# Optimization experiments

Measured on AMD Instinct MI355X. Metric: run time of the kernel, lower is better.

The kernel has to match this reference:

```python
import jax, jax.numpy as jnp
import numpy as np

_SAMPLING_EPS = 1e-5


def setup_inputs() -> dict:
    key = jax.random.key(0)
    k1, k2, k3, k4, k5 = jax.random.split(key, 5)
    B, V = 128, 128000
    logits = jax.random.normal(k1, (B, V), dtype=jnp.float32)
    temperature = jax.random.uniform(k2, (B,), dtype=jnp.float32)  # some rows < eps -> greedy
    top_k = jax.random.randint(k3, (B,), 1, 64, dtype=jnp.int32)   # in [1, 63]
    top_p = jax.random.uniform(k4, (B,), dtype=jnp.float32, minval=0.05, maxval=1.0)
    noise_u = jax.random.uniform(k5, (B, V), dtype=jnp.float32, minval=1e-10, maxval=1.0)
    return {"logits": logits, "temperature": temperature, "top_k": top_k,
            "top_p": top_p, "noise_u": noise_u, "max_num_logprobs": 5}


def _apply_top_k_top_p(logits, k, p):
    # Faithful to vLLM: ascending sort, top-k threshold mask, top-p cumsum mask, scatter back.
    B, V = logits.shape
    order = jnp.argsort(logits, axis=-1)                       # ascending, [B, V]
    logits_sort = jnp.take_along_axis(logits, order, axis=-1)
    neg_inf = jnp.float32(-jnp.inf)
    # top-k: pivot value at position V - k; everything strictly below it -> -inf
    pivot_idx = (V - k.astype(jnp.int32))[:, None]             # [B, 1]
    pivot = jnp.take_along_axis(logits_sort, pivot_idx, axis=-1)
    logits_sort = jnp.where(logits_sort < pivot, neg_inf, logits_sort)
    # top-p: softmax over sorted logits, cumsum, drop prefix with mass <= 1 - p (keep last)
    probs_sort = jax.nn.softmax(logits_sort, axis=-1)
    probs_sum = jnp.cumsum(probs_sort, axis=-1)
    top_p_mask = probs_sum <= (1.0 - p)[:, None]
    top_p_mask = top_p_mask.at[:, -1].set(False)
    logits_sort = jnp.where(top_p_mask, neg_inf, logits_sort)
    # scatter back to original vocab order
    rows = jnp.arange(B)[:, None]
    return jnp.zeros_like(logits).at[rows, order].set(logits_sort)


def reference(logits, temperature, top_k, top_p, noise_u, max_num_logprobs):
    # temperature scaling (temp < eps means greedy; divide by 1.0 instead)
    temp = jnp.where(temperature < _SAMPLING_EPS, 1.0, temperature)
    logits = logits.astype(jnp.float32) / temp[:, None]
    # top-k / top-p filtering
    logits = _apply_top_k_top_p(logits, top_k, top_p)
    # probabilities and sampling
    probs = jax.nn.softmax(logits, axis=-1)
    greedy = jnp.argmax(probs, axis=-1)
    q = -jnp.log(noise_u)                                      # Exp(1) noise (q.exponential_())
    random = jnp.argmax(probs / q, axis=-1)
    sampled = jnp.where(temperature < _SAMPLING_EPS, greedy, random).astype(jnp.int32)
    # top-k logprobs
    logprobs = jax.nn.log_softmax(logits, axis=-1)
    topk_logprobs, topk_indices = jax.lax.top_k(logprobs, max_num_logprobs)
    return sampled, topk_indices.astype(jnp.int32), topk_logprobs
```

## Files before the change

kernel.cpp:

```cpp
#include <hip/hip_runtime.h>
#include <math.h>
#include <stdint.h>

#define BT     256
#define WPB    4
#define TOPC   64
#define CAPW   1024
#define WT     512
#define NSL_HI 32
#define NSL_LO 16
#define NC_MAX (NSL_HI * TOPC)

__device__ __forceinline__ unsigned f2ord(float f) {
    unsigned u = __float_as_uint(f);
    return u ^ ((u & 0x80000000u) ? 0xFFFFFFFFu : 0x80000000u);
}
__device__ __forceinline__ float ord2f(unsigned k) {
    unsigned u = (k & 0x80000000u) ? (k ^ 0x80000000u) : (k ^ 0xFFFFFFFFu);
    return __uint_as_float(u);
}

template<int G>
__device__ unsigned wave_rebuild64_g(unsigned* key, int* idx, unsigned n,
                                     int lane, unsigned* out_vst)
{
    unsigned kr[G]; int ir[G];
    #pragma unroll
    for (int g = 0; g < G; ++g) {
        unsigned i = (unsigned)(g * 64 + lane);
        kr[g] = (i < n) ? key[i] : 0u;
        ir[g] = (i < n) ? idx[i] : 0;
    }
    unsigned p = 0u;
    for (int bit = 31; bit >= 0; --bit) {
        unsigned t = p | (1u << bit);
        int c = 0;
        #pragma unroll
        for (int g = 0; g < G; ++g)
            c += __popcll(__ballot(kr[g] >= t));
        if (c >= TOPC) p = t;
    }
    const unsigned long long ltm = (1ull << lane) - 1ull;
    unsigned c = 0;
    #pragma unroll
    for (int g = 0; g < G; ++g) {
        unsigned i = (unsigned)(g * 64 + lane);
        bool pa = (i < n) && (kr[g] > p);
        unsigned long long m = __ballot(pa);
        if (pa) { unsigned pos = c + (unsigned)__popcll(m & ltm); key[pos] = kr[g]; idx[pos] = ir[g]; }
        c += (unsigned)__popcll(m);
    }
    #pragma unroll
    for (int g = 0; g < G; ++g) {
        unsigned i = (unsigned)(g * 64 + lane);
        bool pa = (i < n) && (kr[g] == p);
        unsigned long long m = __ballot(pa);
        if (pa) {
            unsigned pos = c + (unsigned)__popcll(m & ltm);
            if (pos < TOPC) { key[pos] = kr[g]; idx[pos] = ir[g]; }
        }
        c += (unsigned)__popcll(m);
    }
    *out_vst = p;
    return (c < TOPC) ? c : TOPC;
}

__device__ __forceinline__ unsigned wave_rebuild64(unsigned* key, int* idx,
                                                   unsigned n, int lane,
                                                   unsigned* out_vst)
{
    if (n <= 256)  return wave_rebuild64_g<4>(key, idx, n, lane, out_vst);
    if (n <= 512)  return wave_rebuild64_g<8>(key, idx, n, lane, out_vst);
    return wave_rebuild64_g<16>(key, idx, n, lane, out_vst);
}

__global__ __launch_bounds__(BT) void phase1_topk_slices(
    const float* __restrict__ logits, uint2* __restrict__ cand,
    int V, int slice_len, int nsl)
{
    __shared__ unsigned s_key[WPB][CAPW];
    __shared__ int      s_idx[WPB][CAPW];

    const int row  = blockIdx.y;
    const int tid  = threadIdx.x;
    const int wid  = tid >> 6;
    const int lane = tid & 63;
    const int sl   = blockIdx.x * WPB + wid;
    const int s0   = sl * slice_len;
    int s_end = s0 + slice_len; if (s_end > V) s_end = V;
    const float* rowp = logits + (size_t)row * (size_t)V;
    unsigned* mykey = s_key[wid];
    int*      myidx = s_idx[wid];
    const unsigned long long ltm = (1ull << lane) - 1ull;

    const int  tb0 = s0 + 0 * WT + lane * 8, tb1 = s0 + 1 * WT + lane * 8;
    const int  tb2 = s0 + 2 * WT + lane * 8, tb3 = s0 + 3 * WT + lane * 8;
    const int  tb4 = s0 + 4 * WT + lane * 8, tb5 = s0 + 5 * WT + lane * 8;
    const int  tb6 = s0 + 6 * WT + lane * 8, tb7 = s0 + 7 * WT + lane * 8;
    const bool vt0 = tb0 < s_end, vt1 = tb1 < s_end, vt2 = tb2 < s_end,
               vt3 = tb3 < s_end, vt4 = tb4 < s_end, vt5 = tb5 < s_end,
               vt6 = tb6 < s_end, vt7 = tb7 < s_end;

    float4 sa0 = {}, sb0 = {}, sa1 = {}, sb1 = {};
    if (vt0) { sa0 = *(const float4*)(rowp + tb0); sb0 = *(const float4*)(rowp + tb0 + 4); }
    if (vt1) { sa1 = *(const float4*)(rowp + tb1); sb1 = *(const float4*)(rowp + tb1 + 4); }

    float4 A2 = {}, B2 = {}, A3 = {}, B3 = {};
    float4 A4 = {}, B4 = {}, A5 = {}, B5 = {};
    if (vt2) { A2 = *(const float4*)(rowp + tb2); B2 = *(const float4*)(rowp + tb2 + 4); }
    if (vt3) { A3 = *(const float4*)(rowp + tb3); B3 = *(const float4*)(rowp + tb3 + 4); }
    if (vt4) { A4 = *(const float4*)(rowp + tb4); B4 = *(const float4*)(rowp + tb4 + 4); }
    if (vt5) { A5 = *(const float4*)(rowp + tb5); B5 = *(const float4*)(rowp + tb5 + 4); }

    unsigned k0[8], k1[8];
    if (vt0) {
        k0[0] = f2ord(sa0.x); k0[1] = f2ord(sa0.y); k0[2] = f2ord(sa0.z); k0[3] = f2ord(sa0.w);
        k0[4] = f2ord(sb0.x); k0[5] = f2ord(sb0.y); k0[6] = f2ord(sb0.z); k0[7] = f2ord(sb0.w);
    } else {
        #pragma unroll
        for (int j = 0; j < 8; ++j) k0[j] = 0u;
    }
    if (vt1) {
        k1[0] = f2ord(sa1.x); k1[1] = f2ord(sa1.y); k1[2] = f2ord(sa1.z); k1[3] = f2ord(sa1.w);
        k1[4] = f2ord(sb1.x); k1[5] = f2ord(sb1.y); k1[6] = f2ord(sb1.z); k1[7] = f2ord(sb1.w);
    } else {
        #pragma unroll
        for (int j = 0; j < 8; ++j) k1[j] = 0u;
    }

    unsigned lo = 0u, hi = 0xFFFFu;
    while (lo < hi) {
        unsigned mid = (lo + hi + 1u) >> 1;
        unsigned t = mid << 16;
        int cnt16 = 0;
        #pragma unroll
        for (int j = 0; j < 8; ++j) {
            cnt16 += __popcll(__ballot(k0[j] >= t));
            cnt16 += __popcll(__ballot(k1[j] >= t));
        }
        if (cnt16 >= TOPC) lo = mid; else hi = mid - 1u;
    }
    const unsigned thr = lo << 16;

    unsigned cnt = 0u;
    auto append8 = [&](const unsigned* k, int base, bool valid) {
        #pragma unroll
        for (int j = 0; j < 8; ++j) {
            bool pa = valid && (k[j] >= thr);
            unsigned long long m = __ballot(pa);
            if (pa) {
                unsigned pos = cnt + (unsigned)__popcll(m & ltm);
                if (pos < CAPW) { mykey[pos] = k[j]; myidx[pos] = base + j; }
            }
            cnt += (unsigned)__popcll(m);
        }
    };
    auto conv8 = [&](unsigned* k, const float4& a, const float4& b, bool valid) {
        if (valid) {
            k[0] = f2ord(a.x); k[1] = f2ord(a.y); k[2] = f2ord(a.z); k[3] = f2ord(a.w);
            k[4] = f2ord(b.x); k[5] = f2ord(b.y); k[6] = f2ord(b.z); k[7] = f2ord(b.w);
        } else {
            #pragma unroll
            for (int j = 0; j < 8; ++j) k[j] = 0u;
        }
    };

    append8(k0, tb0, vt0);
    append8(k1, tb1, vt1);

    {
        unsigned kk[8];
        conv8(kk, A2, B2, vt2);
        if (vt6) { A2 = *(const float4*)(rowp + tb6); B2 = *(const float4*)(rowp + tb6 + 4); }
        append8(kk, tb2, vt2);
    }
    {
        unsigned kk[8];
        conv8(kk, A3, B3, vt3);
        if (vt7) { A3 = *(const float4*)(rowp + tb7); B3 = *(const float4*)(rowp + tb7 + 4); }
        append8(kk, tb3, vt3);
    }
    {   unsigned kk[8]; conv8(kk, A4, B4, vt4); append8(kk, tb4, vt4); }
    {   unsigned kk[8]; conv8(kk, A5, B5, vt5); append8(kk, tb5, vt5); }
    {   unsigned kk[8]; conv8(kk, A2, B2, vt6); append8(kk, tb6, vt6); }
    {   unsigned kk[8]; conv8(kk, A3, B3, vt7); append8(kk, tb7, vt7); }

    for (int t = s0 + 8 * WT; t < s_end; t += WT) {
        int bs = t + lane * 8;
        bool v = bs < s_end;
        float4 aa = {}, bb = {};
        if (v) { aa = *(const float4*)(rowp + bs); bb = *(const float4*)(rowp + bs + 4); }
        unsigned kk[8];
        conv8(kk, aa, bb, v);
        append8(kk, bs, v);
    }

    asm volatile("s_waitcnt lgkmcnt(0)" ::: "memory");
    __builtin_amdgcn_sched_barrier(0);
    unsigned n = cnt;

    if (n > CAPW) {
        unsigned vst;
        cnt = wave_rebuild64_g<16>(mykey, myidx, CAPW, lane, &vst);
        for (int t = s0; t < s_end; t += WT) {
            int bs = t + lane * 8;
            bool v = bs < s_end;
            float4 aa = {}, bb = {};
            if (v) { aa = *(const float4*)(rowp + bs); bb = *(const float4*)(rowp + bs + 4); }
            unsigned kk[8];
            conv8(kk, aa, bb, v);
            for (;;) {
                unsigned long long m[8]; unsigned tot = 0u;
                #pragma unroll
                for (int j = 0; j < 8; ++j) {
                    m[j] = __ballot(v && (kk[j] > vst));
                    tot += (unsigned)__popcll(m[j]);
                }
                if (cnt + tot <= CAPW) {
                    unsigned c2 = cnt;
                    #pragma unroll
                    for (int j = 0; j < 8; ++j) {
                        if (v && (kk[j] > vst)) {
                            unsigned pos = c2 + (unsigned)__popcll(m[j] & ltm);
                            mykey[pos] = kk[j]; myidx[pos] = bs + j;
                        }
                        c2 += (unsigned)__popcll(m[j]);
                    }
                    cnt = c2;
                    break;
                }
                asm volatile("s_waitcnt lgkmcnt(0)" ::: "memory");
                __builtin_amdgcn_sched_barrier(0);
                cnt = wave_rebuild64_g<16>(mykey, myidx, cnt, lane, &vst);
            }
        }
        asm volatile("s_waitcnt lgkmcnt(0)" ::: "memory");
        __builtin_amdgcn_sched_barrier(0);
        n = cnt;
    }

    unsigned vfin;
    unsigned c2 = wave_rebuild64(mykey, myidx, n, lane, &vfin);
    asm volatile("s_waitcnt lgkmcnt(0)" ::: "memory");
    __builtin_amdgcn_sched_barrier(0);

    uint2* outp = cand + ((size_t)row * (unsigned)nsl + (unsigned)sl) * TOPC;
    unsigned e = (unsigned)lane;
    uint2 val = (e < c2) ? make_uint2(mykey[e], (unsigned)myidx[e])
                         : make_uint2(0u, 0u);
    outp[e] = val;
}

__device__ unsigned radix_select_compact4(uint2* s_buf, uint2* s_keep,
                                          unsigned (*s_hist)[16], unsigned* p_cnt2,
                                          unsigned n, int tid, int wid)
{
    unsigned prefix = 0u;
    int remaining = TOPC;
    for (int shift = 28; shift >= 0; shift -= 4) {
        if (tid < 64) ((unsigned*)s_hist)[tid] = 0u;
        __syncthreads();
        for (unsigned i = (unsigned)tid; i < n; i += BT) {
            unsigned k = s_buf[i].x;
            bool ing = (shift == 28) || ((k >> (shift + 4)) == (prefix >> (shift + 4)));
            if (ing) atomicAdd(&s_hist[wid][(k >> shift) & 15u], 1u);
        }
        __syncthreads();
        int cum = 0; int b = 0; unsigned hb = 0u;
        for (int bb = 15; bb >= 0; --bb) {
            unsigned h = s_hist[0][bb] + s_hist[1][bb] + s_hist[2][bb] + s_hist[3][bb];
            cum += (int)h;
            if (cum >= remaining) { b = bb; hb = h; break; }
        }
        remaining -= (cum - (int)hb);
        prefix |= ((unsigned)b) << shift;
        __syncthreads();
    }
    if (tid == 0) *p_cnt2 = 0u;
    __syncthreads();
    for (unsigned i = (unsigned)tid; i < n; i += BT) {
        uint2 c = s_buf[i];
        if (c.x > prefix) s_keep[atomicAdd(p_cnt2, 1u)] = c;
    }
    __syncthreads();
    for (unsigned i = (unsigned)tid; i < n; i += BT) {
        uint2 c = s_buf[i];
        if (c.x == prefix) {
            unsigned pos = atomicAdd(p_cnt2, 1u);
            if (pos < TOPC) s_keep[pos] = c;
        }
    }
    __syncthreads();
    return prefix;
}

__global__ __launch_bounds__(BT) void phase2_sample(
    const uint2* __restrict__ cand,
    const float* __restrict__ temperature,
    const int*   __restrict__ top_k,
    const float* __restrict__ top_p,
    const float* __restrict__ noise_u,
    float* __restrict__ out,
    int B, int V, int M, int nc)
{
    __shared__ uint2    s_buf[NC_MAX];
    __shared__ uint2    s_keep[TOPC];
    __shared__ unsigned s_hist[4][16];
    __shared__ unsigned s_cnt2;
    __shared__ float    sval[TOPC], se[TOPC], sq[TOPC];
    __shared__ int      sidx[TOPC];

    const int r   = blockIdx.x;
    const int tid = threadIdx.x;
    const int wid = tid >> 6;

    for (int i = tid; i < nc; i += BT)
        s_buf[i] = cand[(size_t)r * nc + i];
    __syncthreads();
    radix_select_compact4(s_buf, s_keep, s_hist, &s_cnt2, (unsigned)nc, tid, wid);

    for (int kk = 2; kk <= TOPC; kk <<= 1) {
        for (int j = kk >> 1; j > 0; j >>= 1) {
            if (tid < TOPC / 2) {
                int i0 = ((tid & ~(j - 1)) << 1) | (tid & (j - 1));
                int i1 = i0 | j;
                bool up = ((i0 & kk) == 0);
                uint2 A = s_keep[i0], Bv = s_keep[i1];
                bool gt = (A.x < Bv.x) || (A.x == Bv.x && A.y > Bv.y);
                if (gt == up) { s_keep[i0] = Bv; s_keep[i1] = A; }
            }
            __syncthreads();
        }
    }

    float temp_orig = temperature[r];
    float temp = (temp_orig < 1e-5f) ? 1.0f : temp_orig;

    if (tid < TOPC) {
        unsigned k = s_keep[tid].x;
        int id = (int)s_keep[tid].y;
        sval[tid] = ord2f(k) / temp;
        sidx[tid] = id;
        float u = noise_u[(size_t)r * (size_t)V + id];
        sq[tid] = -logf(u);
    }
    __syncthreads();
    if (tid < TOPC) se[tid] = expf(sval[tid] - sval[0]);
    __syncthreads();

    if (tid == 0) {
        int k = top_k[r];
        if (k < 1) k = 1; if (k > TOPC) k = TOPC;
        float p = top_p[r];

        float pivot = sval[k - 1];
        int m = k;
        while (m < TOPC && sval[m] >= pivot) ++m;

        float sum = 0.f;
        for (int i = 0; i < m; ++i) sum += se[i];

        float thr1 = 1.0f - p;
        float S = 0.f;
        int f = 1;
        for (int i = m - 1; i >= 1; --i) {
            S += se[i] / sum;
            if (S > thr1) { f = i + 1; break; }
        }

        float sum2 = 0.f;
        for (int i = 0; i < f; ++i) sum2 += se[i];

        int greedy = sidx[0];
        float best = -1.f; int bidx = 0x7fffffff;
        for (int i = 0; i < f; ++i) {
            float ratio = (se[i] / sum2) / sq[i];
            if (ratio > best || (ratio == best && sidx[i] < bidx)) {
                best = ratio; bidx = sidx[i];
            }
        }
        int sampled = (temp_orig < 1e-5f) ? greedy : bidx;

        float lse = logf(sum2);
        out[r] = (float)sampled;
        float* oidx = out + B + (size_t)r * M;
        float* olp  = out + B + (size_t)B * M + (size_t)r * M;
        int produced = 0;
        for (int i = 0; i < f && produced < M; ++i, ++produced) {
            oidx[produced] = (float)sidx[i];
            olp[produced]  = (sval[i] - sval[0]) - lse;
        }
        int v = 0;
        while (produced < M) {
            bool used = false;
            for (int i = 0; i < f; ++i) if (sidx[i] == v) { used = true; break; }
            if (!used) { oidx[produced] = (float)v; olp[produced] = -3.0e38f; ++produced; }
            ++v;
        }
    }
}

extern "C" void kernel_launch(void* const* d_in, const int* in_sizes, int n_in,
                              void* d_out, int out_size, void* d_ws, size_t ws_size,
                              hipStream_t stream)
{
    const float* logits      = (const float*)d_in[0];
    const float* temperature = (const float*)d_in[1];
    const int*   top_k       = (const int*)d_in[2];
    const float* top_p       = (const float*)d_in[3];
    const float* noise_u     = (const float*)d_in[4];

    const int B = in_sizes[1];
    const int V = in_sizes[0] / B;
    const int M = (out_size / B - 1) / 2;

    const size_t need32 = (size_t)B * NSL_HI * TOPC * sizeof(uint2);
    const int nsl = (ws_size >= need32) ? NSL_HI : NSL_LO;

    uint2* cand = (uint2*)d_ws;

    int slice_len = (((V + nsl - 1) / nsl) + 7) & ~7;

    dim3 g1(nsl / WPB, B);
    phase1_topk_slices<<<g1, BT, 0, stream>>>(logits, cand, V, slice_len, nsl);
    phase2_sample<<<B, BT, 0, stream>>>(cand, temperature, top_k, top_p, noise_u,
                                        (float*)d_out, B, V, M, nsl * TOPC);
}
```

Baseline: 180.0 us.

## Stream logits through an LDS ring with async global-to-LDS loads in phase 1

Phase 1 now pulls each slice through an 8-stage per-wave LDS ring using global_load_lds async copies, with vmcnt waits, instead of register-held float4 prefetches. The aim is to keep more memory requests in flight while the threshold and append work runs. Slice count drops from 32 to 24 and candidate capacity from 1024 to 640, which frees LDS for the ring and shrinks phase-2 input. Some lgkmcnt waits around the rebuilds are removed. This risks hazards between LDS reads and writes, and the larger per-wave slices give less grid parallelism.

```diff
diff --git a/kernel.cpp b/kernel.cpp
--- a/kernel.cpp
+++ b/kernel.cpp
@@ -5,11 +5,13 @@
 #define BT     256
 #define WPB    4
 #define TOPC   64
-#define CAPW   1024
+#define CAPW   640
+#define SUB    256
+#define RING   8
 #define WT     512
-#define NSL_HI 32
-#define NSL_LO 16
-#define NC_MAX (NSL_HI * TOPC)
+#define NSL_HI 24
+#define NSL_LO 8
+#define NC_MAX 2048
 
 __device__ __forceinline__ unsigned f2ord(float f) {
     unsigned u = __float_as_uint(f);
@@ -19,6 +21,14 @@
     unsigned u = (k & 0x80000000u) ? (k ^ 0x80000000u) : (k ^ 0xFFFFFFFFu);
     return __uint_as_float(u);
 }
+
+__device__ __forceinline__ void async_copy16(const float* gsrc, unsigned* lds) {
+    __builtin_amdgcn_global_load_lds(
+        (const __attribute__((address_space(1))) void*)gsrc,
+        (__attribute__((address_space(3))) void*)lds, 16, 0, 0);
+}
+#define WAITV(N) do { asm volatile("s_waitcnt vmcnt(" #N ")" ::: "memory"); \
+                      __builtin_amdgcn_sched_barrier(0); } while (0)
 
 template<int G>
 __device__ unsigned wave_rebuild64_g(unsigned* key, int* idx, unsigned n,
@@ -64,20 +74,20 @@
     *out_vst = p;
     return (c < TOPC) ? c : TOPC;
 }
-
 __device__ __forceinline__ unsigned wave_rebuild64(unsigned* key, int* idx,
                                                    unsigned n, int lane,
                                                    unsigned* out_vst)
 {
-    if (n <= 256)  return wave_rebuild64_g<4>(key, idx, n, lane, out_vst);
-    if (n <= 512)  return wave_rebuild64_g<8>(key, idx, n, lane, out_vst);
-    return wave_rebuild64_g<16>(key, idx, n, lane, out_vst);
+    if (n <= 256) return wave_rebuild64_g<4>(key, idx, n, lane, out_vst);
+    if (n <= 512) return wave_rebuild64_g<8>(key, idx, n, lane, out_vst);
+    return wave_rebuild64_g<12>(key, idx, n, lane, out_vst);
 }
 
 __global__ __launch_bounds__(BT) void phase1_topk_slices(
     const float* __restrict__ logits, uint2* __restrict__ cand,
     int V, int slice_len, int nsl)
 {
+    __shared__ unsigned s_ring[WPB][RING * SUB];
     __shared__ unsigned s_key[WPB][CAPW];
     __shared__ int      s_idx[WPB][CAPW];
 
@@ -89,64 +99,65 @@
     const int s0   = sl * slice_len;
     int s_end = s0 + slice_len; if (s_end > V) s_end = V;
     const float* rowp = logits + (size_t)row * (size_t)V;
+    unsigned* ring  = s_ring[wid];
     unsigned* mykey = s_key[wid];
     int*      myidx = s_idx[wid];
     const unsigned long long ltm = (1ull << lane) - 1ull;
-
-    const int  tb0 = s0 + 0 * WT + lane * 8, tb1 = s0 + 1 * WT + lane * 8;
-    const int  tb2 = s0 + 2 * WT + lane * 8, tb3 = s0 + 3 * WT + lane * 8;
-    const int  tb4 = s0 + 4 * WT + lane * 8, tb5 = s0 + 5 * WT + lane * 8;
-    const int  tb6 = s0 + 6 * WT + lane * 8, tb7 = s0 + 7 * WT + lane * 8;
-    const bool vt0 = tb0 < s_end, vt1 = tb1 < s_end, vt2 = tb2 < s_end,
-               vt3 = tb3 < s_end, vt4 = tb4 < s_end, vt5 = tb5 < s_end,
-               vt6 = tb6 < s_end, vt7 = tb7 < s_end;
-
-    float4 sa0 = {}, sb0 = {}, sa1 = {}, sb1 = {};
-    if (vt0) { sa0 = *(const float4*)(rowp + tb0); sb0 = *(const float4*)(rowp + tb0 + 4); }
-    if (vt1) { sa1 = *(const float4*)(rowp + tb1); sb1 = *(const float4*)(rowp + tb1 + 4); }
-
-    float4 A2 = {}, B2 = {}, A3 = {}, B3 = {};
-    float4 A4 = {}, B4 = {}, A5 = {}, B5 = {};
-    if (vt2) { A2 = *(const float4*)(rowp + tb2); B2 = *(const float4*)(rowp + tb2 + 4); }
-    if (vt3) { A3 = *(const float4*)(rowp + tb3); B3 = *(const float4*)(rowp + tb3 + 4); }
-    if (vt4) { A4 = *(const float4*)(rowp + tb4); B4 = *(const float4*)(rowp + tb4 + 4); }
-    if (vt5) { A5 = *(const float4*)(rowp + tb5); B5 = *(const float4*)(rowp + tb5 + 4); }
-
-    unsigned k0[8], k1[8];
-    if (vt0) {
-        k0[0] = f2ord(sa0.x); k0[1] = f2ord(sa0.y); k0[2] = f2ord(sa0.z); k0[3] = f2ord(sa0.w);
-        k0[4] = f2ord(sb0.x); k0[5] = f2ord(sb0.y); k0[6] = f2ord(sb0.z); k0[7] = f2ord(sb0.w);
-    } else {
-        #pragma unroll
-        for (int j = 0; j < 8; ++j) k0[j] = 0u;
-    }
-    if (vt1) {
-        k1[0] = f2ord(sa1.x); k1[1] = f2ord(sa1.y); k1[2] = f2ord(sa1.z); k1[3] = f2ord(sa1.w);
-        k1[4] = f2ord(sb1.x); k1[5] = f2ord(sb1.y); k1[6] = f2ord(sb1.z); k1[7] = f2ord(sb1.w);
-    } else {
-        #pragma unroll
-        for (int j = 0; j < 8; ++j) k1[j] = 0u;
+    const int lane4 = lane * 4;
+
+    uint2* outp = cand + ((size_t)row * (unsigned)nsl + (unsigned)sl) * TOPC;
+
+    const int NSUB = (s_end > s0) ? ((s_end - s0 + SUB - 1) / SUB) : 0;
+    if (NSUB <= 0) {
+        outp[lane] = make_uint2(0u, 0u);
+        return;
+    }
+    const int vclamp = V - 4;
+
+    auto issue = [&](int st) {
+        int off = s0 + st * SUB + lane4;
+        const float* g = rowp + ((off <= vclamp) ? off : vclamp);
+        async_copy16(g, &ring[(st & (RING - 1)) * SUB]);
+    };
+
+    const int ni0 = (NSUB < RING) ? NSUB : RING;
+    for (int st = 0; st < ni0; ++st) issue(st);
+    int issued = ni0;
+
+    const int sseed = (NSUB < 4) ? NSUB : 4;
+    if (NSUB >= RING) { WAITV(4); } else { WAITV(0); }
+
+    unsigned kr[16];
+    #pragma unroll
+    for (int st = 0; st < 4; ++st) {
+        if (st < sseed) {
+            uint4 r = *(const uint4*)(&ring[st * SUB + lane4]);
+            kr[st * 4 + 0] = f2ord(__uint_as_float(r.x));
+            kr[st * 4 + 1] = f2ord(__uint_as_float(r.y));
+            kr[st * 4 + 2] = f2ord(__uint_as_float(r.z));
+            kr[st * 4 + 3] = f2ord(__uint_as_float(r.w));
+        } else {
+            kr[st * 4 + 0] = 0u; kr[st * 4 + 1] = 0u;
+            kr[st * 4 + 2] = 0u; kr[st * 4 + 3] = 0u;
+        }
     }
 
     unsigned lo = 0u, hi = 0xFFFFu;
     while (lo < hi) {
         unsigned mid = (lo + hi + 1u) >> 1;
         unsigned t = mid << 16;
-        int cnt16 = 0;
+        int c16 = 0;
         #pragma unroll
-        for (int j = 0; j < 8; ++j) {
-            cnt16 += __popcll(__ballot(k0[j] >= t));
-            cnt16 += __popcll(__ballot(k1[j] >= t));
-        }
-        if (cnt16 >= TOPC) lo = mid; else hi = mid - 1u;
+        for (int j = 0; j < 16; ++j) c16 += __popcll(__ballot(kr[j] >= t));
+        if (c16 >= TOPC) lo = mid; else hi = mid - 1u;
     }
     const unsigned thr = lo << 16;
 
     unsigned cnt = 0u;
-    auto append8 = [&](const unsigned* k, int base, bool valid) {
+    auto append4 = [&](const unsigned* k, int base) {
         #pragma unroll
-        for (int j = 0; j < 8; ++j) {
-            bool pa = valid && (k[j] >= thr);
+        for (int j = 0; j < 4; ++j) {
+            bool pa = (base + j < s_end) && (k[j] >= thr);
             unsigned long long m = __ballot(pa);
             if (pa) {
                 unsigned pos = cnt + (unsigned)__popcll(m & ltm);
@@ -155,60 +166,53 @@
             cnt += (unsigned)__popcll(m);
         }
     };
-    auto conv8 = [&](unsigned* k, const float4& a, const float4& b, bool valid) {
-        if (valid) {
-            k[0] = f2ord(a.x); k[1] = f2ord(a.y); k[2] = f2ord(a.z); k[3] = f2ord(a.w);
-            k[4] = f2ord(b.x); k[5] = f2ord(b.y); k[6] = f2ord(b.z); k[7] = f2ord(b.w);
-        } else {
-            #pragma unroll
-            for (int j = 0; j < 8; ++j) k[j] = 0u;
-        }
-    };
-
-    append8(k0, tb0, vt0);
-    append8(k1, tb1, vt1);
+
+    #pragma unroll
+    for (int st = 0; st < 4; ++st)
+        if (st < sseed) append4(&kr[st * 4], s0 + st * SUB + lane4);
 
     {
-        unsigned kk[8];
-        conv8(kk, A2, B2, vt2);
-        if (vt6) { A2 = *(const float4*)(rowp + tb6); B2 = *(const float4*)(rowp + tb6 + 4); }
-        append8(kk, tb2, vt2);
-    }
-    {
-        unsigned kk[8];
-        conv8(kk, A3, B3, vt3);
-        if (vt7) { A3 = *(const float4*)(rowp + tb7); B3 = *(const float4*)(rowp + tb7 + 4); }
-        append8(kk, tb3, vt3);
-    }
-    {   unsigned kk[8]; conv8(kk, A4, B4, vt4); append8(kk, tb4, vt4); }
-    {   unsigned kk[8]; conv8(kk, A5, B5, vt5); append8(kk, tb5, vt5); }
-    {   unsigned kk[8]; conv8(kk, A2, B2, vt6); append8(kk, tb6, vt6); }
-    {   unsigned kk[8]; conv8(kk, A3, B3, vt7); append8(kk, tb7, vt7); }
-
-    for (int t = s0 + 8 * WT; t < s_end; t += WT) {
-        int bs = t + lane * 8;
-        bool v = bs < s_end;
-        float4 aa = {}, bb = {};
-        if (v) { aa = *(const float4*)(rowp + bs); bb = *(const float4*)(rowp + bs + 4); }
-        unsigned kk[8];
-        conv8(kk, aa, bb, v);
-        append8(kk, bs, v);
-    }
-
-    asm volatile("s_waitcnt lgkmcnt(0)" ::: "memory");
-    __builtin_amdgcn_sched_barrier(0);
+        const int tgt = (NSUB < sseed + RING) ? NSUB : (sseed + RING);
+        for (; issued < tgt; ++issued) issue(issued);
+    }
+
+    int i = sseed;
+    for (; i + RING < NSUB; ++i) {
+        WAITV(7);
+        uint4 r = *(const uint4*)(&ring[(i & (RING - 1)) * SUB + lane4]);
+        unsigned kk[4];
+        kk[0] = f2ord(__uint_as_float(r.x)); kk[1] = f2ord(__uint_as_float(r.y));
+        kk[2] = f2ord(__uint_as_float(r.z)); kk[3] = f2ord(__uint_as_float(r.w));
+        issue(i + RING); ++issued;
+        append4(kk, s0 + i * SUB + lane4);
+    }
+    WAITV(0);
+    for (; i < NSUB; ++i) {
+        uint4 r = *(const uint4*)(&ring[(i & (RING - 1)) * SUB + lane4]);
+        unsigned kk[4];
+        kk[0] = f2ord(__uint_as_float(r.x)); kk[1] = f2ord(__uint_as_float(r.y));
+        kk[2] = f2ord(__uint_as_float(r.z)); kk[3] = f2ord(__uint_as_float(r.w));
+        append4(kk, s0 + i * SUB + lane4);
+    }
+
     unsigned n = cnt;
 
     if (n > CAPW) {
         unsigned vst;
-        cnt = wave_rebuild64_g<16>(mykey, myidx, CAPW, lane, &vst);
+        cnt = wave_rebuild64_g<12>(mykey, myidx, CAPW, lane, &vst);
         for (int t = s0; t < s_end; t += WT) {
             int bs = t + lane * 8;
             bool v = bs < s_end;
             float4 aa = {}, bb = {};
             if (v) { aa = *(const float4*)(rowp + bs); bb = *(const float4*)(rowp + bs + 4); }
             unsigned kk[8];
-            conv8(kk, aa, bb, v);
+            if (v) {
+                kk[0] = f2ord(aa.x); kk[1] = f2ord(aa.y); kk[2] = f2ord(aa.z); kk[3] = f2ord(aa.w);
+                kk[4] = f2ord(bb.x); kk[5] = f2ord(bb.y); kk[6] = f2ord(bb.z); kk[7] = f2ord(bb.w);
+            } else {
+                #pragma unroll
+                for (int j = 0; j < 8; ++j) kk[j] = 0u;
+            }
             for (;;) {
                 unsigned long long m[8]; unsigned tot = 0u;
                 #pragma unroll
@@ -229,26 +233,18 @@
                     cnt = c2;
                     break;
                 }
-                asm volatile("s_waitcnt lgkmcnt(0)" ::: "memory");
-                __builtin_amdgcn_sched_barrier(0);
-                cnt = wave_rebuild64_g<16>(mykey, myidx, cnt, lane, &vst);
+                cnt = wave_rebuild64_g<12>(mykey, myidx, cnt, lane, &vst);
             }
         }
-        asm volatile("s_waitcnt lgkmcnt(0)" ::: "memory");
-        __builtin_amdgcn_sched_barrier(0);
         n = cnt;
     }
 
     unsigned vfin;
     unsigned c2 = wave_rebuild64(mykey, myidx, n, lane, &vfin);
-    asm volatile("s_waitcnt lgkmcnt(0)" ::: "memory");
-    __builtin_amdgcn_sched_barrier(0);
-
-    uint2* outp = cand + ((size_t)row * (unsigned)nsl + (unsigned)sl) * TOPC;
-    unsigned e = (unsigned)lane;
-    uint2 val = (e < c2) ? make_uint2(mykey[e], (unsigned)myidx[e])
-                         : make_uint2(0u, 0u);
-    outp[e] = val;
+    uint2 val = ((unsigned)lane < c2)
+              ? make_uint2(mykey[lane], (unsigned)myidx[lane])
+              : make_uint2(0u, 0u);
+    outp[lane] = val;
 }
 
 __device__ unsigned radix_select_compact4(uint2* s_buf, uint2* s_keep,
@@ -414,12 +410,12 @@
     const int V = in_sizes[0] / B;
     const int M = (out_size / B - 1) / 2;
 
-    const size_t need32 = (size_t)B * NSL_HI * TOPC * sizeof(uint2);
-    const int nsl = (ws_size >= need32) ? NSL_HI : NSL_LO;
+    const size_t needHI = (size_t)B * NSL_HI * TOPC * sizeof(uint2);
+    const int nsl = (ws_size >= needHI) ? NSL_HI : NSL_LO;
 
     uint2* cand = (uint2*)d_ws;
 
-    int slice_len = (((V + nsl - 1) / nsl) + 7) & ~7;
+    int slice_len = (((V + nsl - 1) / nsl) + SUB - 1) & ~(SUB - 1);
 
     dim3 g1(nsl / WPB, B);
     phase1_topk_slices<<<g1, BT, 0, stream>>>(logits, cand, V, slice_len, nsl);
```

Measured after the change: 174.4 us. 3.1% less time.
